# Kernel optimization log

Measured on AMD Instinct MI355X. Metric: run time of the kernel, lower is better.

## Reference

```python
import jax, jax.numpy as jnp
import numpy as np

# so(3) generators (3x3x3), L[s, r, a]
L = jnp.array([[[0, 0, 0], [0, 0, -1], [0, 1, 0]],
               [[0, 0, 1], [0, 0, 0], [-1, 0, 0]],
               [[0, -1, 0], [1, 0, 0], [0, 0, 0]]], dtype=jnp.float32)


def setup_inputs() -> dict:
    key = jax.random.key(0)
    B, S, X, Y = 32, 3, 512, 512
    s = jax.random.normal(key, (B, S, X, Y), dtype=jnp.float32)
    # normalize to unit O(3) spins (physically realistic; math identical for any s)
    s = s / jnp.linalg.norm(s, axis=1, keepdims=True)
    t = jnp.ones((1,), dtype=jnp.float32)   # flow time
    c0 = jnp.ones((1,), dtype=jnp.float32)  # learnable coefficient C[0]
    return {"s": s, "t": t, "c0": c0}


def reference(s, t, c0):
    # Psi11t.grad(s, t): flow force of the (psi_1^1)^2 action term.
    # Coeff(t) with EvenOdd=False and cc=[c0] is t * c0.
    coeff = t * c0  # shape [1], broadcasts

    def nbr(x, mu):
        # sum of forward and backward periodic neighbors along lattice axis mu
        return jnp.roll(x, -1, axis=mu) + jnp.roll(x, 1, axis=mu)

    # b[b,x,y] = sum_mu s . (s shifted +/- along mu)
    b = (jnp.einsum('bsxy,bsxy->bxy', s, nbr(s, 2))
         + jnp.einsum('bsxy,bsxy->bxy', s, nbr(s, 3)))

    bs = s * b[:, None]  # [B,3,X,Y]

    # Lsig[b,r,a,x,y] = -sum_s s[b,s,x,y] * L[s,r,a]
    Lsig = -jnp.einsum('bsxy,sra->braxy', s, L)

    Fs = nbr(s, 2) + nbr(s, 3)      # [B,3,X,Y]
    Fbs = nbr(bs, 2) + nbr(bs, 3)   # [B,3,X,Y]

    F = Fs * b[:, None] + Fbs
    F = jnp.einsum('bsaxy,bsxy->baxy', Lsig, F)  # so(3) generator contraction
    return 2.0 * coeff * F
```

## Files before the change

### kernel.cpp

```cpp
#include <hip/hip_runtime.h>

#define BATCH 32
#define NX 512
#define NY 512
#define XY (NX * NY)

typedef float floatx4 __attribute__((ext_vector_type(4)));

__global__ __launch_bounds__(256, 2) void psi11t_kernel(
    const float* __restrict__ s,
    const float* __restrict__ t,
    const float* __restrict__ c0,
    float* __restrict__ out)
{
    const int D = blockIdx.x;
    const int L = (D & 7) * 512 + (D >> 3);
    const int bidx  = L >> 7;
    const int strip = L & 127;

    const int tid = threadIdx.x;
    const int yg  = tid & 127;
    const int xr  = tid >> 7;
    const int y0  = yg * 4;
    const int x   = strip * 4 + xr * 2;

    const int xm2 = (x + NX - 2) & (NX - 1);
    const int xm1 = (x + NX - 1) & (NX - 1);
    const int xp1 = x + 1;
    const int xp2 = (x + 2) & (NX - 1);
    const int xp3 = (x + 3) & (NX - 1);
    const int om4 = (y0 + NY - 4) & (NY - 1);
    const int op4 = (y0 + 4)      & (NY - 1);

    const float* sb = s + (size_t)bidx * 3 * XY;

    float A2m[3][4], Am[3][12], C0[3][12], C1[3][12], Bp[3][12], B2p[3][4];

    #pragma unroll
    for (int c = 0; c < 3; ++c) {
        const float* base = sb + (size_t)c * XY;
        const float* rm2 = base + (size_t)xm2 * NY;
        const float* rm1 = base + (size_t)xm1 * NY;
        const float* r0  = base + (size_t)x   * NY;
        const float* r1  = base + (size_t)xp1 * NY;
        const float* rp2 = base + (size_t)xp2 * NY;
        const float* rp3 = base + (size_t)xp3 * NY;

        *(floatx4*)&A2m[c][0] = *(const floatx4*)(rm2 + y0);
        *(floatx4*)&Am[c][0]  = *(const floatx4*)(rm1 + om4);
        *(floatx4*)&Am[c][4]  = *(const floatx4*)(rm1 + y0);
        *(floatx4*)&Am[c][8]  = *(const floatx4*)(rm1 + op4);
        *(floatx4*)&C0[c][0]  = *(const floatx4*)(r0 + om4);
        *(floatx4*)&C0[c][4]  = *(const floatx4*)(r0 + y0);
        *(floatx4*)&C0[c][8]  = *(const floatx4*)(r0 + op4);
        *(floatx4*)&C1[c][0]  = *(const floatx4*)(r1 + om4);
        *(floatx4*)&C1[c][4]  = *(const floatx4*)(r1 + y0);
        *(floatx4*)&C1[c][8]  = *(const floatx4*)(r1 + op4);
        *(floatx4*)&Bp[c][0]  = *(const floatx4*)(rp2 + om4);
        *(floatx4*)&Bp[c][4]  = *(const floatx4*)(rp2 + y0);
        *(floatx4*)&Bp[c][8]  = *(const floatx4*)(rp2 + op4);
        *(floatx4*)&B2p[c][0] = *(const floatx4*)(rp3 + y0);
    }

    const float coeff = 2.0f * t[0] * c0[0];

    float b0[6], b1[6], bm[4], bp2[4];

    #pragma unroll
    for (int j = 0; j < 6; ++j) {
        float a0 = 0.f, a1 = 0.f;
        #pragma unroll
        for (int c = 0; c < 3; ++c) {
            a0 += C0[c][3 + j] * (Am[c][3 + j] + C1[c][3 + j] + C0[c][2 + j] + C0[c][4 + j]);
            a1 += C1[c][3 + j] * (C0[c][3 + j] + Bp[c][3 + j] + C1[c][2 + j] + C1[c][4 + j]);
        }
        b0[j] = a0;
        b1[j] = a1;
    }
    #pragma unroll
    for (int i = 0; i < 4; ++i) {
        float am = 0.f, ap = 0.f;
        #pragma unroll
        for (int c = 0; c < 3; ++c) {
            am += Am[c][4 + i] * (A2m[c][i] + C0[c][4 + i] + Am[c][3 + i] + Am[c][5 + i]);
            ap += Bp[c][4 + i] * (C1[c][4 + i] + B2p[c][i] + Bp[c][3 + i] + Bp[c][5 + i]);
        }
        bm[i]  = am;
        bp2[i] = ap;
    }

    float o0[3][4], o1[3][4];
    #pragma unroll
    for (int i = 0; i < 4; ++i) {
        float G0[3], G1[3];
        #pragma unroll
        for (int c = 0; c < 3; ++c) {
            float Fs0 = Am[c][4 + i] + C1[c][4 + i] + C0[c][3 + i] + C0[c][5 + i];
            G0[c] = Fs0 * b0[1 + i]
                  + Am[c][4 + i] * bm[i]
                  + C1[c][4 + i] * b1[1 + i]
                  + C0[c][3 + i] * b0[i]
                  + C0[c][5 + i] * b0[2 + i];
            float Fs1 = C0[c][4 + i] + Bp[c][4 + i] + C1[c][3 + i] + C1[c][5 + i];
            G1[c] = Fs1 * b1[1 + i]
                  + C0[c][4 + i] * b0[1 + i]
                  + Bp[c][4 + i] * bp2[i]
                  + C1[c][3 + i] * b1[i]
                  + C1[c][5 + i] * b1[2 + i];
        }
        o0[0][i] = (C0[1][4 + i] * G0[2] - C0[2][4 + i] * G0[1]) * coeff;
        o0[1][i] = (C0[2][4 + i] * G0[0] - C0[0][4 + i] * G0[2]) * coeff;
        o0[2][i] = (C0[0][4 + i] * G0[1] - C0[1][4 + i] * G0[0]) * coeff;
        o1[0][i] = (C1[1][4 + i] * G1[2] - C1[2][4 + i] * G1[1]) * coeff;
        o1[1][i] = (C1[2][4 + i] * G1[0] - C1[0][4 + i] * G1[2]) * coeff;
        o1[2][i] = (C1[0][4 + i] * G1[1] - C1[1][4 + i] * G1[0]) * coeff;
    }

    float* ob = out + (size_t)bidx * 3 * XY + (size_t)x * NY + y0;
    #pragma unroll
    for (int c = 0; c < 3; ++c) {
        floatx4 v0 = { o0[c][0], o0[c][1], o0[c][2], o0[c][3] };
        floatx4 v1 = { o1[c][0], o1[c][1], o1[c][2], o1[c][3] };
        __builtin_nontemporal_store(v0, (floatx4*)(ob + (size_t)c * XY));
        __builtin_nontemporal_store(v1, (floatx4*)(ob + (size_t)c * XY + NY));
    }
}

extern "C" void kernel_launch(void* const* d_in, const int* in_sizes, int n_in,
                              void* d_out, int out_size, void* d_ws, size_t ws_size,
                              hipStream_t stream) {
    const float* s  = (const float*)d_in[0];
    const float* t  = (const float*)d_in[1];
    const float* c0 = (const float*)d_in[2];
    float* out = (float*)d_out;

    psi11t_kernel<<<4096, 256, 0, stream>>>(s, t, c0, out);
}
```

Measured before the change: 191.8 us.

## Stage spin rows and b-field in LDS to remove redundant global loads

Rewrites the stencil so each 512-thread block loads six halo rows of all three spin components into shared memory once. It computes the b field for those rows into a second LDS buffer and then evaluates the force from LDS with one output row per thread. This replaces the per-thread redundant global loads and duplicated b recomputation of the register-only version. The cost is two block barriers, about 48KB of LDS per block, and a different occupancy (512 threads, launch bound 6).

```diff
diff --git a/kernel.cpp b/kernel.cpp
--- a/kernel.cpp
+++ b/kernel.cpp
@@ -1,129 +1,136 @@
 #include <hip/hip_runtime.h>
 
-#define BATCH 32
 #define NX 512
 #define NY 512
 #define XY (NX * NY)
 
-typedef float floatx4 __attribute__((ext_vector_type(4)));
+typedef float f4 __attribute__((ext_vector_type(4)));
 
-__global__ __launch_bounds__(256, 2) void psi11t_kernel(
+__global__ __launch_bounds__(512, 6) void psi11t_kernel(
     const float* __restrict__ s,
     const float* __restrict__ t,
     const float* __restrict__ c0,
     float* __restrict__ out)
 {
+    __shared__ __align__(16) float s_lds[3 * 6 * NY];
+    __shared__ __align__(16) float b_lds[6 * NY];
+
     const int D = blockIdx.x;
     const int L = (D & 7) * 512 + (D >> 3);
     const int bidx  = L >> 7;
     const int strip = L & 127;
-
+    const int x0  = strip * 4;
     const int tid = threadIdx.x;
-    const int yg  = tid & 127;
-    const int xr  = tid >> 7;
-    const int y0  = yg * 4;
-    const int x   = strip * 4 + xr * 2;
-
-    const int xm2 = (x + NX - 2) & (NX - 1);
-    const int xm1 = (x + NX - 1) & (NX - 1);
-    const int xp1 = x + 1;
-    const int xp2 = (x + 2) & (NX - 1);
-    const int xp3 = (x + 3) & (NX - 1);
-    const int om4 = (y0 + NY - 4) & (NY - 1);
-    const int op4 = (y0 + 4)      & (NY - 1);
+    const int y4g = tid & 127;
+    const int yb  = y4g * 4;
 
     const float* sb = s + (size_t)bidx * 3 * XY;
 
-    float A2m[3][4], Am[3][12], C0[3][12], C1[3][12], Bp[3][12], B2p[3][4];
+    auto ldchunk = [&](int k) -> f4 {
+        const int rl = k >> 7;
+        const int c  = rl / 6;
+        const int r  = rl - 6 * c;
+        const int xg = (x0 - 1 + r) & (NX - 1);
+        return *(const f4*)(sb + (size_t)c * XY + (size_t)xg * NY + (k & 127) * 4);
+    };
+    f4 st0 = ldchunk(tid);
+    f4 st1 = ldchunk(tid + 512);
+    f4 st2 = ldchunk(tid + 1024);
+    f4 st3 = ldchunk(tid + 1536);
+    f4 st4;
+    if (tid < 256) st4 = ldchunk(tid + 2048);
 
+    f4 ge[3];
+    if (tid < 256) {
+        const int xe = (tid < 128) ? ((x0 - 2) & (NX - 1)) : ((x0 + 5) & (NX - 1));
+        const float* re = sb + (size_t)xe * NY + yb;
+        #pragma unroll
+        for (int c = 0; c < 3; ++c) ge[c] = *(const f4*)(re + (size_t)c * XY);
+    }
+
+    *(f4*)&s_lds[(size_t)tid * 4]          = st0;
+    *(f4*)&s_lds[(size_t)(tid + 512) * 4]  = st1;
+    *(f4*)&s_lds[(size_t)(tid + 1024) * 4] = st2;
+    *(f4*)&s_lds[(size_t)(tid + 1536) * 4] = st3;
+    if (tid < 256) *(f4*)&s_lds[(size_t)(tid + 2048) * 4] = st4;
+    __syncthreads();
+
+    const int ym = (yb + NY - 1) & (NY - 1);
+    const int yp = (yb + 4) & (NY - 1);
+
+    {
+        const int rb = tid >> 7;
+        f4 acc = {0.f, 0.f, 0.f, 0.f};
+        #pragma unroll
+        for (int c = 0; c < 3; ++c) {
+            const float* Sc = &s_lds[(c * 6 + rb) * NY];
+            f4 ce = *(const f4*)(Sc + yb);
+            f4 up;
+            if (rb == 0) up = ge[c];
+            else         up = *(const f4*)(Sc - NY + yb);
+            f4 dn = *(const f4*)(Sc + NY + yb);
+            float lf = Sc[ym], rt = Sc[yp];
+            f4 shl = {lf, ce[0], ce[1], ce[2]};
+            f4 shr = {ce[1], ce[2], ce[3], rt};
+            acc += ce * (up + dn + shl + shr);
+        }
+        *(f4*)&b_lds[rb * NY + yb] = acc;
+    }
+    if (tid < 256) {
+        const int rb = 4 + (tid >> 7);
+        f4 acc = {0.f, 0.f, 0.f, 0.f};
+        #pragma unroll
+        for (int c = 0; c < 3; ++c) {
+            const float* Sc = &s_lds[(c * 6 + rb) * NY];
+            f4 ce = *(const f4*)(Sc + yb);
+            f4 up = *(const f4*)(Sc - NY + yb);
+            f4 dn;
+            if (rb == 5) dn = ge[c];
+            else         dn = *(const f4*)(Sc + NY + yb);
+            float lf = Sc[ym], rt = Sc[yp];
+            f4 shl = {lf, ce[0], ce[1], ce[2]};
+            f4 shr = {ce[1], ce[2], ce[3], rt};
+            acc += ce * (up + dn + shl + shr);
+        }
+        *(f4*)&b_lds[rb * NY + yb] = acc;
+    }
+    __syncthreads();
+
+    const int r = tid >> 7;
+    const int x = x0 + r;
+
+    const float* Bc = &b_lds[(r + 1) * NY];
+    f4 bc = *(const f4*)(Bc + yb);
+    f4 bu = *(const f4*)(Bc - NY + yb);
+    f4 bd = *(const f4*)(Bc + NY + yb);
+    float bl = Bc[ym], br = Bc[yp];
+    f4 bshl = {bl, bc[0], bc[1], bc[2]};
+    f4 bshr = {bc[1], bc[2], bc[3], br};
+
+    f4 G[3], cen[3];
     #pragma unroll
     for (int c = 0; c < 3; ++c) {
-        const float* base = sb + (size_t)c * XY;
-        const float* rm2 = base + (size_t)xm2 * NY;
-        const float* rm1 = base + (size_t)xm1 * NY;
-        const float* r0  = base + (size_t)x   * NY;
-        const float* r1  = base + (size_t)xp1 * NY;
-        const float* rp2 = base + (size_t)xp2 * NY;
-        const float* rp3 = base + (size_t)xp3 * NY;
-
-        *(floatx4*)&A2m[c][0] = *(const floatx4*)(rm2 + y0);
-        *(floatx4*)&Am[c][0]  = *(const floatx4*)(rm1 + om4);
-        *(floatx4*)&Am[c][4]  = *(const floatx4*)(rm1 + y0);
-        *(floatx4*)&Am[c][8]  = *(const floatx4*)(rm1 + op4);
-        *(floatx4*)&C0[c][0]  = *(const floatx4*)(r0 + om4);
-        *(floatx4*)&C0[c][4]  = *(const floatx4*)(r0 + y0);
-        *(floatx4*)&C0[c][8]  = *(const floatx4*)(r0 + op4);
-        *(floatx4*)&C1[c][0]  = *(const floatx4*)(r1 + om4);
-        *(floatx4*)&C1[c][4]  = *(const floatx4*)(r1 + y0);
-        *(floatx4*)&C1[c][8]  = *(const floatx4*)(r1 + op4);
-        *(floatx4*)&Bp[c][0]  = *(const floatx4*)(rp2 + om4);
-        *(floatx4*)&Bp[c][4]  = *(const floatx4*)(rp2 + y0);
-        *(floatx4*)&Bp[c][8]  = *(const floatx4*)(rp2 + op4);
-        *(floatx4*)&B2p[c][0] = *(const floatx4*)(rp3 + y0);
+        const float* Sc = &s_lds[(c * 6 + r + 1) * NY];
+        f4 ce = *(const f4*)(Sc + yb);
+        f4 up = *(const f4*)(Sc - NY + yb);
+        f4 dn = *(const f4*)(Sc + NY + yb);
+        float lf = Sc[ym], rt = Sc[yp];
+        f4 shl = {lf, ce[0], ce[1], ce[2]};
+        f4 shr = {ce[1], ce[2], ce[3], rt};
+        f4 Fs = up + dn + shl + shr;
+        G[c] = Fs * bc + up * bu + dn * bd + shl * bshl + shr * bshr;
+        cen[c] = ce;
     }
 
     const float coeff = 2.0f * t[0] * c0[0];
+    f4 o0 = (cen[1] * G[2] - cen[2] * G[1]) * coeff;
+    f4 o1 = (cen[2] * G[0] - cen[0] * G[2]) * coeff;
+    f4 o2 = (cen[0] * G[1] - cen[1] * G[0]) * coeff;
 
-    float b0[6], b1[6], bm[4], bp2[4];
-
-    #pragma unroll
-    for (int j = 0; j < 6; ++j) {
-        float a0 = 0.f, a1 = 0.f;
-        #pragma unroll
-        for (int c = 0; c < 3; ++c) {
-            a0 += C0[c][3 + j] * (Am[c][3 + j] + C1[c][3 + j] + C0[c][2 + j] + C0[c][4 + j]);
-            a1 += C1[c][3 + j] * (C0[c][3 + j] + Bp[c][3 + j] + C1[c][2 + j] + C1[c][4 + j]);
-        }
-        b0[j] = a0;
-        b1[j] = a1;
-    }
-    #pragma unroll
-    for (int i = 0; i < 4; ++i) {
-        float am = 0.f, ap = 0.f;
-        #pragma unroll
-        for (int c = 0; c < 3; ++c) {
-            am += Am[c][4 + i] * (A2m[c][i] + C0[c][4 + i] + Am[c][3 + i] + Am[c][5 + i]);
-            ap += Bp[c][4 + i] * (C1[c][4 + i] + B2p[c][i] + Bp[c][3 + i] + Bp[c][5 + i]);
-        }
-        bm[i]  = am;
-        bp2[i] = ap;
-    }
-
-    float o0[3][4], o1[3][4];
-    #pragma unroll
-    for (int i = 0; i < 4; ++i) {
-        float G0[3], G1[3];
-        #pragma unroll
-        for (int c = 0; c < 3; ++c) {
-            float Fs0 = Am[c][4 + i] + C1[c][4 + i] + C0[c][3 + i] + C0[c][5 + i];
-            G0[c] = Fs0 * b0[1 + i]
-                  + Am[c][4 + i] * bm[i]
-                  + C1[c][4 + i] * b1[1 + i]
-                  + C0[c][3 + i] * b0[i]
-                  + C0[c][5 + i] * b0[2 + i];
-            float Fs1 = C0[c][4 + i] + Bp[c][4 + i] + C1[c][3 + i] + C1[c][5 + i];
-            G1[c] = Fs1 * b1[1 + i]
-                  + C0[c][4 + i] * b0[1 + i]
-                  + Bp[c][4 + i] * bp2[i]
-                  + C1[c][3 + i] * b1[i]
-                  + C1[c][5 + i] * b1[2 + i];
-        }
-        o0[0][i] = (C0[1][4 + i] * G0[2] - C0[2][4 + i] * G0[1]) * coeff;
-        o0[1][i] = (C0[2][4 + i] * G0[0] - C0[0][4 + i] * G0[2]) * coeff;
-        o0[2][i] = (C0[0][4 + i] * G0[1] - C0[1][4 + i] * G0[0]) * coeff;
-        o1[0][i] = (C1[1][4 + i] * G1[2] - C1[2][4 + i] * G1[1]) * coeff;
-        o1[1][i] = (C1[2][4 + i] * G1[0] - C1[0][4 + i] * G1[2]) * coeff;
-        o1[2][i] = (C1[0][4 + i] * G1[1] - C1[1][4 + i] * G1[0]) * coeff;
-    }
-
-    float* ob = out + (size_t)bidx * 3 * XY + (size_t)x * NY + y0;
-    #pragma unroll
-    for (int c = 0; c < 3; ++c) {
-        floatx4 v0 = { o0[c][0], o0[c][1], o0[c][2], o0[c][3] };
-        floatx4 v1 = { o1[c][0], o1[c][1], o1[c][2], o1[c][3] };
-        __builtin_nontemporal_store(v0, (floatx4*)(ob + (size_t)c * XY));
-        __builtin_nontemporal_store(v1, (floatx4*)(ob + (size_t)c * XY + NY));
-    }
+    float* ob = out + (size_t)bidx * 3 * XY + (size_t)x * NY + yb;
+    __builtin_nontemporal_store(o0, (f4*)ob);
+    __builtin_nontemporal_store(o1, (f4*)(ob + XY));
+    __builtin_nontemporal_store(o2, (f4*)(ob + 2 * XY));
 }
 
 extern "C" void kernel_launch(void* const* d_in, const int* in_sizes, int n_in,
@@ -134,5 +141,5 @@
     const float* c0 = (const float*)d_in[2];
     float* out = (float*)d_out;
 
-    psi11t_kernel<<<4096, 256, 0, stream>>>(s, t, c0, out);
+    psi11t_kernel<<<4096, 512, 0, stream>>>(s, t, c0, out);
 }
```

Measured after the change: 179.5 us. -6.4%, faster.
